# Optimization experiments

Measured on AMD Instinct MI355X. Metric: run time of the kernel, lower is better.

## Reference

```python
import jax, jax.numpy as jnp
import numpy as np
import math

K = 3
K2 = 9
BANDS = 8

def _linear(x, w, b):
    return x @ w.T + b

def _gelu(x):
    return jax.nn.gelu(x, approximate=False)

def setup_inputs() -> dict:
    key = jax.random.key(0)
    ks = jax.random.split(key, 14)
    def p(k, shape):
        return jax.random.normal(k, shape, dtype=jnp.float32) * 0.05
    inp = {
        "feat": jax.random.normal(ks[0], (2, 64, 128, 128), dtype=jnp.float32),
        "w1m": p(ks[1], (64, 85)),  "b1m": p(ks[2], (64,)),
        "w2m": p(ks[3], (64, 64)),  "b2m": p(ks[4], (64,)),
        "wk1": p(ks[5], (128, 640)), "bk1": p(ks[6], (128,)),
        "wk2": p(ks[7], (9, 128)),   "bk2": p(ks[8], (9,)),
        "wr1": p(ks[9], (64, 64)),   "br1": p(ks[10], (64,)),
        "wr2": p(ks[11], (3, 64)),   "br2": p(ks[12], (3,)),
        "scale": 2,
    }
    return inp

def reference(feat, w1m, b1m, w2m, b2m, wk1, bk1, wk2, bk2, wr1, br1, wr2, br2, scale):
    B, C, H, W = feat.shape
    s = float(scale)
    oh = max(1, int(round(H * s)))
    ow = max(1, int(round(W * s)))
    kappa = max(0.1, 1.0 / s)
    eta = min(1.0, 0.15 * s)
    pad = K // 2

    # ---- query geometry (shared across batch: uniform scale) ----
    ys = jnp.arange(oh, dtype=feat.dtype)
    xs = jnp.arange(ow, dtype=feat.dtype)
    yy, xx = jnp.meshgrid(ys, xs, indexing='ij')
    src_y = (yy + 0.5) / s - 0.5
    src_x = (xx + 0.5) / s - 0.5
    cell_y = jnp.floor(src_y)
    cell_x = jnp.floor(src_x)
    du = (src_x - cell_x - 0.5).reshape(-1)  # (q,)
    dv = (src_y - cell_y - 0.5).reshape(-1)
    q = oh * ow

    # ---- gather local KxK patches (replicates unfold + index_select) ----
    cy = jnp.clip(cell_y, 0, H - 1).astype(jnp.int32).reshape(-1)
    cx = jnp.clip(cell_x, 0, W - 1).astype(jnp.int32).reshape(-1)
    padded = jnp.pad(feat, ((0, 0), (0, 0), (pad, pad), (pad, pad)), mode='reflect')
    off = jnp.arange(K, dtype=jnp.int32)
    rows = cy[:, None] + off                 # (q, K) -> padded row indices
    cols = cx[:, None] + off                 # (q, K)
    # (B, C, q, K, K)
    g = padded[:, :, rows[:, :, None], cols[:, None, :]]
    g = jnp.transpose(g, (0, 2, 1, 3, 4)).reshape(B, q, C * K2)  # torch unfold layout (c, kh, kw)
    # torch does gathered.view(q, k2, c) on the channel-major flat -> faithful reshape
    patches = g.reshape(B, q, K2, C)
    patches_flat = g  # (B, q, C*K2), identical to patches.reshape(q, -1)

    # ---- meta fourier encoding + meta MLP (shared across batch) ----
    m = jnp.stack([
        jnp.full((q,), s, dtype=feat.dtype),
        du, dv,
        jnp.full((q,), kappa, dtype=feat.dtype),
        jnp.full((q,), eta, dtype=feat.dtype),
    ], axis=1)                               # (q, 5)
    freqs = (2.0 ** jnp.arange(BANDS, dtype=feat.dtype)) * math.pi
    xb = m[..., None] * freqs                # (q, 5, BANDS)
    enc = jnp.concatenate([m[..., None], jnp.sin(xb), jnp.cos(xb)], axis=-1).reshape(q, -1)  # (q, 85)
    m_emb = _linear(_gelu(_linear(enc, w1m, b1m)), w2m, b2m)  # (q, channels)

    # ---- kernel generation + softmax-weighted aggregate ----
    m_emb_b = jnp.broadcast_to(m_emb[None], (B, q, m_emb.shape[-1]))
    kin = jnp.concatenate([patches_flat, m_emb_b], axis=-1)   # (B, q, 640)
    weights = _linear(_gelu(_linear(kin, wk1, bk1)), wk2, bk2)  # (B, q, K2)
    weights = jax.nn.softmax(weights, axis=-1)
    f_q = jnp.einsum('bqk,bqkc->bqc', weights, patches)       # (B, q, C)

    # ---- rgb head ----
    rgb = _linear(_gelu(_linear(f_q, wr1, br1)), wr2, br2)    # (B, q, 3)
    rgb = rgb.reshape(B, oh, ow, -1).transpose(0, 3, 1, 2)    # (B, 3, oh, ow)
    return rgb
```

## Files before the change

kernel.cpp:

```cpp
#include <hip/hip_runtime.h>
#include <math.h>

#define HH 128
#define WW 128

typedef __attribute__((ext_vector_type(8))) short s16x8;
typedef __attribute__((ext_vector_type(8))) _Float16 h16x8;
typedef __attribute__((ext_vector_type(4))) float f32x4;

__device__ __forceinline__ float gelu_f(float x){
    return 0.5f * x * (1.0f + erff(x * 0.70710678118654752440f));
}
__device__ __forceinline__ float gelu_fast(float x){
    const float u2 = 1.5957691216057308f * x * (1.0f + 0.044715f * x * x);
    const float e  = __expf(u2);
    const float t  = 1.0f - 2.0f / (e + 1.0f);
    return 0.5f * x * (1.0f + t);
}
__device__ __forceinline__ int refl(int v, int n){
    return v < 0 ? -v : (v >= n ? 2*n - 2 - v : v);
}
__device__ __forceinline__ ushort f2bf(float f){
    unsigned int b = __float_as_uint(f);
    unsigned int r = (b + 0x7FFFu + ((b >> 16) & 1u)) >> 16;
    return (ushort)r;
}
__device__ __forceinline__ float bf2f(ushort u){
    return __uint_as_float(((unsigned int)u) << 16);
}

__global__ __launch_bounds__(256) void featTp_kernel(
    const float* __restrict__ feat, ushort* __restrict__ featTp)
{
    const int i = blockIdx.x * 256 + threadIdx.x;
    if (i >= 270400) return;
    const int cb  = i & 7;
    const int col = (i >> 3) % 130;
    const int row = (i / 1040) % 130;
    const int b   = i / 135200;

    const int sr = refl(row - 1, HH);
    const int sc = refl(col - 1, WW);
    const float* __restrict__ src = feat + ((size_t)(b*64 + cb*8) << 14) + (sr << 7) + sc;
    ushort tmp[8];
    #pragma unroll
    for (int j = 0; j < 8; ++j) tmp[j] = f2bf(src[(size_t)j << 14]);
    ushort* dst = featTp + ((((size_t)b*130 + row)*130 + col) << 6) + cb*8;
    *(int4*)dst = *(const int4*)tmp;
}

__global__ __launch_bounds__(256) void prep_all(
    const float* __restrict__ w1m, const float* __restrict__ b1m,
    const float* __restrict__ w2m, const float* __restrict__ b2m,
    const float* __restrict__ wk1, const float* __restrict__ bk1,
    const float* __restrict__ wr1,
    float* __restrict__ contrib, ushort* __restrict__ wk1tap,
    _Float16* __restrict__ wr1h)
{
    const int blk = blockIdx.x;
    const int t = threadIdx.x;

    if (blk == 0){
        __shared__ float hs[4][64];
        __shared__ float m_emb[4][64];
        const int p = t >> 6;
        const int j = t & 63;

        const float du = (p & 1) ? -0.25f : 0.25f;
        const float dv = (p >> 1) ? -0.25f : 0.25f;
        const float mv[5] = {2.0f, du, dv, 0.5f, 0.3f};

        float enc[85];
        #pragma unroll
        for (int f = 0; f < 5; ++f){
            enc[f*17] = mv[f];
            float fr = 3.14159265358979323846f;
            #pragma unroll
            for (int b = 0; b < 8; ++b){
                float xb = mv[f] * fr;
                enc[f*17 + 1 + b] = sinf(xb);
                enc[f*17 + 9 + b] = cosf(xb);
                fr *= 2.0f;
            }
        }

        float h = b1m[j];
        const float* __restrict__ wrow = w1m + j*85;
        #pragma unroll
        for (int i = 0; i < 85; ++i) h += enc[i] * wrow[i];
        hs[p][j] = gelu_f(h);
        __syncthreads();

        {
            const int o = j;
            float acc = b2m[o];
            const float* __restrict__ w2row = w2m + o*64;
            #pragma unroll
            for (int jj = 0; jj < 64; ++jj) acc += hs[p][jj] * w2row[jj];
            m_emb[p][o] = acc;
        }
        __syncthreads();

        for (int e = t; e < 512; e += 256){
            const int pp = e >> 7;
            const int oo = e & 127;
            float a = bk1[oo];
            #pragma unroll
            for (int jj = 0; jj < 64; ++jj) a += m_emb[pp][jj] * wk1[oo*640 + 576 + jj];
            contrib[e] = a;
        }
    } else if (blk <= 288){
        const int i = (blk - 1)*256 + t;
        if (i < 73728){
            const int c   = i & 63;
            const int o   = (i >> 6) & 127;
            const int tap = i >> 13;
            wk1tap[i] = f2bf(wk1[o*640 + c*9 + tap]);
        }
    } else {
        const int i = (blk - 289)*256 + t;
        if (i < 8192) wr1h[i] = (_Float16)wr1[i];
    }
}

__global__ __launch_bounds__(512) void conv_kernel(
    const ushort* __restrict__ featTp,
    const ushort* __restrict__ wk1tap,
    const float* __restrict__ wk2, const float* __restrict__ bk2,
    const float* __restrict__ contrib,
    _Float16* __restrict__ fqh)
{
    __shared__ ushort As[4*34*64];
    __shared__ float  Ls[64][129];
    __shared__ float  wk2s[1152];
    __shared__ float  w9s[256*9];
    __shared__ ushort tbl[576];

    const int t   = threadIdx.x;
    const int blk = blockIdx.x;
    const int b   = blk >> 8;
    const int rem = blk & 255;
    const int cy0 = (rem >> 2) * 2;
    const int cx0 = (rem & 3) * 32;

    for (int e = t; e < 1088; e += 512){
        const int r   = e / 272;
        const int rm  = e - r * 272;
        const int col = rm >> 3;
        const int cb  = rm & 7;
        const ushort* src = featTp + ((((size_t)b*130 + cy0 + r)*130 + cx0 + col) << 6) + cb*8;
        const int didx = (r*34 + col)*64 + ((cb ^ (col & 7)) << 3);
        *(int4*)&As[didx] = *(const int4*)src;
    }
    for (int e = t; e < 1152; e += 512) wk2s[e] = wk2[e];
    for (int e = t; e < 576; e += 512){
        const int ch  = e / 9;
        const int tap = e - 9*ch;
        const int ty  = tap / 3;
        const int tx  = tap - 3*ty;
        tbl[e] = (ushort)((ch << 9) | ((ty*34 + tx) << 2) | tx);
    }
    __syncthreads();

    {
        const int lane = t & 63;
        const int w    = t >> 6;
        const int wn   = w & 1;
        const int wq   = w >> 1;
        const int cellrow = wq >> 1;
        const int colblk  = (wq & 1) * 16;
        const int l15  = lane & 15;
        const int l4   = lane >> 4;

        f32x4 acc[4];
        #pragma unroll
        for (int n = 0; n < 4; ++n) acc[n] = (f32x4){0.f,0.f,0.f,0.f};

        const int acol = colblk + l15;

        #pragma unroll
        for (int tap = 0; tap < 9; ++tap){
            const int ky = tap / 3;
            const int kx = tap - ky * 3;

            s16x8 bf[2][4];
            #pragma unroll
            for (int ks = 0; ks < 2; ++ks)
                #pragma unroll
                for (int n = 0; n < 4; ++n)
                    bf[ks][n] = *(const s16x8*)(wk1tap +
                        (((size_t)tap << 13) + ((wn*64 + n*16 + l15) << 6) + ks*32 + l4*8));

            const int col = acol + kx;
            const int rowbase = (cellrow + ky)*34 + col;
            const int sw = (col & 7);
            #pragma unroll
            for (int ks = 0; ks < 2; ++ks){
                const int cb0 = ks*4 + l4;
                const s16x8 af = *(const s16x8*)&As[rowbase*64 + ((cb0 ^ sw) << 3)];
                #pragma unroll
                for (int n = 0; n < 4; ++n)
                    acc[n] = __builtin_amdgcn_mfma_f32_16x16x32_bf16(af, bf[ks][n], acc[n], 0, 0, 0);
            }
        }

        #pragma unroll
        for (int n = 0; n < 4; ++n){
            #pragma unroll
            for (int reg = 0; reg < 4; ++reg){
                const int lc = cellrow*32 + colblk + l4*4 + reg;
                const int o  = wn*64 + n*16 + l15;
                Ls[lc][o] = acc[n][reg];
            }
        }
    }
    __syncthreads();

    {
        const int task = t >> 1;
        const int half = t & 1;
        const int lc   = task >> 2;
        const int p    = task & 3;

        float w9[9];
        #pragma unroll
        for (int k = 0; k < 9; ++k) w9[k] = 0.0f;

        const int rot = (p*16 + half*8) & 63;
        for (int ii = 0; ii < 64; ++ii){
            const int o = half*64 + ((rot + ii) & 63);
            const float h = gelu_fast(Ls[lc][o] + contrib[p*128 + o]);
            #pragma unroll
            for (int k = 0; k < 9; ++k) w9[k] += wk2s[k*128 + o] * h;
        }
        #pragma unroll
        for (int k = 0; k < 9; ++k) w9[k] += __shfl_xor(w9[k], 1);
        #pragma unroll
        for (int k = 0; k < 9; ++k) w9[k] += bk2[k];

        float mx = w9[0];
        #pragma unroll
        for (int k = 1; k < 9; ++k) mx = fmaxf(mx, w9[k]);
        float sum = 0.0f;
        #pragma unroll
        for (int k = 0; k < 9; ++k){ w9[k] = __expf(w9[k] - mx); sum += w9[k]; }
        const float inv = 1.0f / sum;
        #pragma unroll
        for (int k = 0; k < 9; ++k) w9[k] *= inv;

        if (half == 0){
            w9s[task*9+0] = w9[0]; w9s[task*9+1] = w9[1]; w9s[task*9+2] = w9[2];
            w9s[task*9+3] = w9[3]; w9s[task*9+4] = w9[4];
        } else {
            w9s[task*9+5] = w9[5]; w9s[task*9+6] = w9[6];
            w9s[task*9+7] = w9[7]; w9s[task*9+8] = w9[8];
        }
    }
    __syncthreads();

    {
        const int ci  = t >> 3;
        const int sub = t & 7;
        const int rr  = ci >> 5;
        const int x   = ci & 31;
        const int base_rc = rr*34 + x;
        const int c0 = sub*8;

        float w9r[4][9];
        #pragma unroll
        for (int p = 0; p < 4; ++p)
            #pragma unroll
            for (int k = 0; k < 9; ++k)
                w9r[p][k] = w9s[(ci*4 + p)*9 + k];

        float fqa[4][8];
        #pragma unroll
        for (int p = 0; p < 4; ++p)
            #pragma unroll
            for (int i = 0; i < 8; ++i) fqa[p][i] = 0.0f;

        #pragma unroll
        for (int k = 0; k < 9; ++k){
            #pragma unroll
            for (int i = 0; i < 8; ++i){
                const int e  = tbl[k*64 + c0 + i];
                const int tx = e & 3;
                const int rc = (e >> 2) & 127;
                const int ch = e >> 9;
                const int col = x + tx;
                const int aidx = ((base_rc + rc) << 6)
                               + (((ch >> 3) ^ (col & 7)) << 3) + (ch & 7);
                const float v = bf2f(As[aidx]);
                fqa[0][i] += w9r[0][k] * v;
                fqa[1][i] += w9r[1][k] * v;
                fqa[2][i] += w9r[2][k] * v;
                fqa[3][i] += w9r[3][k] * v;
            }
        }

        const int gy = cy0 + rr;
        const int gx = cx0 + x;

        #pragma unroll
        for (int p = 0; p < 4; ++p){
            const int py = p >> 1, px = p & 1;
            h16x8 hv;
            #pragma unroll
            for (int i = 0; i < 8; ++i) hv[i] = (_Float16)fqa[p][i];

            const int oy0 = 2*gy + 2 - py;
            const int ox0 = 2*gx + 2 - px;
            const bool y0ok = (py == 1) || (gy < 127);
            const bool x0ok = (px == 1) || (gx < 127);
            const bool yEx  = (gy == 0) && (py == 0);
            const bool xEx  = (gx == 0) && (px == 0);

            if (y0ok && x0ok)
                *(h16x8*)(fqh + (((size_t)((b << 16) | (oy0 << 8) | ox0)) << 6) + c0) = hv;
            if (y0ok && xEx)
                *(h16x8*)(fqh + (((size_t)((b << 16) | (oy0 << 8))) << 6) + c0) = hv;
            if (yEx && x0ok)
                *(h16x8*)(fqh + (((size_t)((b << 16) | ox0)) << 6) + c0) = hv;
            if (yEx && xEx)
                *(h16x8*)(fqh + (((size_t)(b << 16)) << 6) + c0) = hv;
        }
    }
}

__global__ __launch_bounds__(256) void rgb_kernel(
    const _Float16* __restrict__ fqh,
    const _Float16* __restrict__ wr1h,
    const float* __restrict__ br1, const float* __restrict__ wr2,
    const float* __restrict__ br2,
    float* __restrict__ out)
{
    const int t    = threadIdx.x;
    const int w    = t >> 6;
    const int lane = t & 63;
    const int l15  = lane & 15;
    const int l4   = lane >> 4;
    const int rowbase = blockIdx.x*64 + w*16;

    const h16x8 a0 = *(const h16x8*)&fqh[(size_t)(rowbase + l15)*64 + l4*8];
    const h16x8 a1 = *(const h16x8*)&fqh[(size_t)(rowbase + l15)*64 + 32 + l4*8];

    f32x4 acc[4];
    #pragma unroll
    for (int n = 0; n < 4; ++n){
        const h16x8 b0 = *(const h16x8*)&wr1h[(n*16 + l15)*64 + l4*8];
        const h16x8 b1 = *(const h16x8*)&wr1h[(n*16 + l15)*64 + 32 + l4*8];
        acc[n] = (f32x4){0.f,0.f,0.f,0.f};
        acc[n] = __builtin_amdgcn_mfma_f32_16x16x32_f16(a0, b0, acc[n], 0, 0, 0);
        acc[n] = __builtin_amdgcn_mfma_f32_16x16x32_f16(a1, b1, acc[n], 0, 0, 0);
    }

    f32x4 br1v, wv0, wv1, wv2;
    #pragma unroll
    for (int n = 0; n < 4; ++n){
        const int col = n*16 + l15;
        br1v[n] = br1[col];
        wv0[n]  = wr2[col];
        wv1[n]  = wr2[64 + col];
        wv2[n]  = wr2[128 + col];
    }
    const float b2r0 = br2[0], b2r1 = br2[1], b2r2 = br2[2];

    #pragma unroll
    for (int reg = 0; reg < 4; ++reg){
        float r0 = 0.f, r1 = 0.f, r2 = 0.f;
        #pragma unroll
        for (int n = 0; n < 4; ++n){
            const float h = gelu_fast(acc[n][reg] + br1v[n]);
            r0 += h * wv0[n];
            r1 += h * wv1[n];
            r2 += h * wv2[n];
        }
        r0 += __shfl_xor(r0, 1); r0 += __shfl_xor(r0, 2); r0 += __shfl_xor(r0, 4); r0 += __shfl_xor(r0, 8);
        r1 += __shfl_xor(r1, 1); r1 += __shfl_xor(r1, 2); r1 += __shfl_xor(r1, 4); r1 += __shfl_xor(r1, 8);
        r2 += __shfl_xor(r2, 1); r2 += __shfl_xor(r2, 2); r2 += __shfl_xor(r2, 4); r2 += __shfl_xor(r2, 8);

        if (l15 == 0){
            const int row = rowbase + l4*4 + reg;
            const int b   = row >> 16;
            const int pix = row & 65535;
            out[((size_t)(b*3 + 0) << 16) + pix] = r0 + b2r0;
            out[((size_t)(b*3 + 1) << 16) + pix] = r1 + b2r1;
            out[((size_t)(b*3 + 2) << 16) + pix] = r2 + b2r2;
        }
    }
}

__global__ __launch_bounds__(256) void main_kernel_mono(
    const float* __restrict__ feat,
    const float* __restrict__ wk1,
    const float* __restrict__ wk2, const float* __restrict__ bk2,
    const float* __restrict__ wr1, const float* __restrict__ br1,
    const float* __restrict__ wr2, const float* __restrict__ br2,
    const float* __restrict__ contrib,
    float* __restrict__ out)
{
    const int tid = blockIdx.x * 256 + threadIdx.x;
    const int b  = tid >> 16;
    const int qi = tid & 65535;
    const int oy = qi >> 8;
    const int ox = qi & 255;

    int cy = (oy - 1) >> 1; if (cy < 0) cy = 0;
    int cx = (ox - 1) >> 1; if (cx < 0) cx = 0;

    int ry[3], rx[3];
    #pragma unroll
    for (int k = 0; k < 3; ++k){ ry[k] = refl(cy-1+k, HH); rx[k] = refl(cx-1+k, WW); }

    const int p = ((oy & 1) << 1) | (ox & 1);
    const float* __restrict__ fb = feat + ((size_t)b << 20);

    float w9[9];
    #pragma unroll
    for (int k = 0; k < 9; ++k) w9[k] = bk2[k];

    for (int oc = 0; oc < 4; ++oc){
        float acc[32];
        #pragma unroll
        for (int j = 0; j < 32; ++j) acc[j] = contrib[p*128 + oc*32 + j];
        for (int c = 0; c < 64; ++c){
            const float* __restrict__ fc = fb + c * (HH*WW);
            float v[9];
            #pragma unroll
            for (int ky = 0; ky < 3; ++ky){
                const float* __restrict__ frow = fc + ry[ky] * WW;
                #pragma unroll
                for (int kx = 0; kx < 3; ++kx) v[ky*3 + kx] = frow[rx[kx]];
            }
            const float* __restrict__ wrow0 = wk1 + (oc*32) * 640 + c * 9;
            #pragma unroll
            for (int j = 0; j < 32; ++j){
                const float* __restrict__ wrow = wrow0 + j * 640;
                float a = acc[j];
                #pragma unroll
                for (int kk = 0; kk < 9; ++kk) a += v[kk] * wrow[kk];
                acc[j] = a;
            }
        }
        #pragma unroll
        for (int j = 0; j < 32; ++j){
            const float h = gelu_f(acc[j]);
            const int o = oc*32 + j;
            #pragma unroll
            for (int k = 0; k < 9; ++k) w9[k] += h * wk2[k*128 + o];
        }
    }

    float mx = w9[0];
    #pragma unroll
    for (int k = 1; k < 9; ++k) mx = fmaxf(mx, w9[k]);
    float sum = 0.0f;
    #pragma unroll
    for (int k = 0; k < 9; ++k){ w9[k] = expf(w9[k] - mx); sum += w9[k]; }
    const float inv = 1.0f / sum;
    #pragma unroll
    for (int k = 0; k < 9; ++k) w9[k] *= inv;

    float fq[64];
    #pragma unroll
    for (int c = 0; c < 64; ++c){
        float a = 0.0f;
        #pragma unroll
        for (int k = 0; k < 9; ++k){
            const int j  = k*64 + c;
            const int ch = j / 9;
            const int kk = j % 9;
            a += w9[k] * fb[ch*(HH*WW) + ry[kk/3]*WW + rx[kk%3]];
        }
        fq[c] = a;
    }

    float r0 = br2[0], r1 = br2[1], r2 = br2[2];
    for (int o = 0; o < 64; ++o){
        float a = br1[o];
        #pragma unroll
        for (int c = 0; c < 64; ++c) a += fq[c] * wr1[o*64 + c];
        const float h = gelu_f(a);
        r0 += h * wr2[o];
        r1 += h * wr2[64 + o];
        r2 += h * wr2[128 + o];
    }

    const int pix = (oy << 8) | ox;
    out[((size_t)(b*3 + 0) << 16) + pix] = r0;
    out[((size_t)(b*3 + 1) << 16) + pix] = r1;
    out[((size_t)(b*3 + 2) << 16) + pix] = r2;
}

extern "C" void kernel_launch(void* const* d_in, const int* in_sizes, int n_in,
                              void* d_out, int out_size, void* d_ws, size_t ws_size,
                              hipStream_t stream)
{
    const float* feat = (const float*)d_in[0];
    const float* w1m  = (const float*)d_in[1];
    const float* b1m  = (const float*)d_in[2];
    const float* w2m  = (const float*)d_in[3];
    const float* b2m  = (const float*)d_in[4];
    const float* wk1  = (const float*)d_in[5];
    const float* bk1  = (const float*)d_in[6];
    const float* wk2  = (const float*)d_in[7];
    const float* bk2  = (const float*)d_in[8];
    const float* wr1  = (const float*)d_in[9];
    const float* br1  = (const float*)d_in[10];
    const float* wr2  = (const float*)d_in[11];
    const float* br2  = (const float*)d_in[12];

    float* out = (float*)d_out;

    char* ws = (char*)d_ws;
    float*     contrib = (float*)ws;
    ushort*    wk1tap  = (ushort*)(ws + 8192);
    _Float16*  wr1h    = (_Float16*)(ws + 155648);
    ushort*    featTp  = (ushort*)(ws + 172032);
    _Float16*  fqh     = (_Float16*)(ws + 4498432);
    const size_t need = 21275648;

    hipLaunchKernelGGL(prep_all, dim3(321), dim3(256), 0, stream,
                       w1m, b1m, w2m, b2m, wk1, bk1, wr1, contrib, wk1tap, wr1h);

    if (ws_size >= need){
        hipLaunchKernelGGL(featTp_kernel, dim3(1057), dim3(256), 0, stream, feat, featTp);
        hipLaunchKernelGGL(conv_kernel, dim3(512), dim3(512), 0, stream,
                           featTp, wk1tap, wk2, bk2, contrib, fqh);
        hipLaunchKernelGGL(rgb_kernel, dim3(2048), dim3(256), 0, stream,
                           fqh, wr1h, br1, wr2, br2, out);
    } else {
        hipLaunchKernelGGL(main_kernel_mono, dim3(512), dim3(256), 0, stream,
                           feat, wk1, wk2, bk2, wr1, br1, wr2, br2, contrib, out);
    }
}
```

Measured before the change: 184.5 us.

## Tile featTp transpose through LDS and restructure conv kernel epilogue stages

The pad/transpose kernel now stages one padded row of all 64 channels in shared memory, so global reads are coalesced along columns, and then writes channel-packed bf16 vectors. The launch shrinks from 1057 to 260 blocks. In the conv kernel, the hidden activations are stored to LDS as fp16 to cut LDS footprint, and wk2 is transposed so each step loads it as float4 vectors. The 9-tap reduction now uses 256 threads, one per query, with no shuffle. The tap lookup table is replaced by multiply-shift index arithmetic, and divisions in GELU and softmax use hardware reciprocal. The trade-offs are lower precision in the intermediate activations and only half the threads active in the softmax stage.

```diff
diff --git a/kernel.cpp b/kernel.cpp
--- a/kernel.cpp
+++ b/kernel.cpp
@@ -11,10 +11,10 @@
 __device__ __forceinline__ float gelu_f(float x){
     return 0.5f * x * (1.0f + erff(x * 0.70710678118654752440f));
 }
-__device__ __forceinline__ float gelu_fast(float x){
+__device__ __forceinline__ float gelu2(float x){
     const float u2 = 1.5957691216057308f * x * (1.0f + 0.044715f * x * x);
     const float e  = __expf(u2);
-    const float t  = 1.0f - 2.0f / (e + 1.0f);
+    const float t  = 1.0f - 2.0f * __builtin_amdgcn_rcpf(e + 1.0f);
     return 0.5f * x * (1.0f + t);
 }
 __device__ __forceinline__ int refl(int v, int n){
@@ -32,21 +32,36 @@
 __global__ __launch_bounds__(256) void featTp_kernel(
     const float* __restrict__ feat, ushort* __restrict__ featTp)
 {
-    const int i = blockIdx.x * 256 + threadIdx.x;
-    if (i >= 270400) return;
-    const int cb  = i & 7;
-    const int col = (i >> 3) % 130;
-    const int row = (i / 1040) % 130;
-    const int b   = i / 135200;
-
-    const int sr = refl(row - 1, HH);
-    const int sc = refl(col - 1, WW);
-    const float* __restrict__ src = feat + ((size_t)(b*64 + cb*8) << 14) + (sr << 7) + sc;
-    ushort tmp[8];
-    #pragma unroll
-    for (int j = 0; j < 8; ++j) tmp[j] = f2bf(src[(size_t)j << 14]);
-    ushort* dst = featTp + ((((size_t)b*130 + row)*130 + col) << 6) + cb*8;
-    *(int4*)dst = *(const int4*)tmp;
+    __shared__ ushort tile[64*132];
+
+    const int blk = blockIdx.x;
+    const int b   = blk / 130;
+    const int row = blk - b*130;
+    const int sr  = refl(row - 1, HH);
+
+    const int c2   = threadIdx.x >> 7;
+    const int scol = threadIdx.x & 127;
+
+    #pragma unroll 4
+    for (int cc = 0; cc < 32; ++cc){
+        const int c = cc*2 + c2;
+        const float v = feat[(((size_t)(b*64 + c)) << 14) + (sr << 7) + scol];
+        const ushort bv = f2bf(v);
+        tile[c*132 + scol + 1] = bv;
+        if (scol == 1)   tile[c*132 + 0]   = bv;
+        if (scol == 126) tile[c*132 + 129] = bv;
+    }
+    __syncthreads();
+
+    for (int e = threadIdx.x; e < 1040; e += 256){
+        const int col = e >> 3;
+        const int cb  = e & 7;
+        ushort tmp[8];
+        #pragma unroll
+        for (int j = 0; j < 8; ++j) tmp[j] = tile[(cb*8 + j)*132 + col];
+        *(int4*)(featTp + ((((size_t)b*130 + row)*130 + col) << 6) + cb*8)
+            = *(const int4*)tmp;
+    }
 }
 
 __global__ __launch_bounds__(256) void prep_all(
@@ -131,10 +146,10 @@
     _Float16* __restrict__ fqh)
 {
     __shared__ ushort As[4*34*64];
-    __shared__ float  Ls[64][129];
-    __shared__ float  wk2s[1152];
-    __shared__ float  w9s[256*9];
-    __shared__ ushort tbl[576];
+    __shared__ ushort Ls16[64*130];
+    __shared__ float  wk2t[128*12];
+    __shared__ float  w9s[256*10];
+    __shared__ float  contribs[512];
 
     const int t   = threadIdx.x;
     const int blk = blockIdx.x;
@@ -152,14 +167,12 @@
         const int didx = (r*34 + col)*64 + ((cb ^ (col & 7)) << 3);
         *(int4*)&As[didx] = *(const int4*)src;
     }
-    for (int e = t; e < 1152; e += 512) wk2s[e] = wk2[e];
-    for (int e = t; e < 576; e += 512){
-        const int ch  = e / 9;
-        const int tap = e - 9*ch;
-        const int ty  = tap / 3;
-        const int tx  = tap - 3*ty;
-        tbl[e] = (ushort)((ch << 9) | ((ty*34 + tx) << 2) | tx);
-    }
+    for (int e = t; e < 1536; e += 512){
+        const int o = (e * 10923) >> 17;
+        const int k = e - o*12;
+        if (k < 9) wk2t[e] = wk2[k*128 + o];
+    }
+    if (t < 512) contribs[t] = contrib[t];
     __syncthreads();
 
     {
@@ -210,31 +223,30 @@
             for (int reg = 0; reg < 4; ++reg){
                 const int lc = cellrow*32 + colblk + l4*4 + reg;
                 const int o  = wn*64 + n*16 + l15;
-                Ls[lc][o] = acc[n][reg];
+                Ls16[lc*130 + o] = __builtin_bit_cast(ushort, (_Float16)acc[n][reg]);
             }
         }
     }
     __syncthreads();
 
-    {
-        const int task = t >> 1;
-        const int half = t & 1;
-        const int lc   = task >> 2;
-        const int p    = task & 3;
+    if (t < 256){
+        const int cell = t & 63;
+        const int p    = t >> 6;
 
         float w9[9];
         #pragma unroll
         for (int k = 0; k < 9; ++k) w9[k] = 0.0f;
 
-        const int rot = (p*16 + half*8) & 63;
-        for (int ii = 0; ii < 64; ++ii){
-            const int o = half*64 + ((rot + ii) & 63);
-            const float h = gelu_fast(Ls[lc][o] + contrib[p*128 + o]);
-            #pragma unroll
-            for (int k = 0; k < 9; ++k) w9[k] += wk2s[k*128 + o] * h;
-        }
-        #pragma unroll
-        for (int k = 0; k < 9; ++k) w9[k] += __shfl_xor(w9[k], 1);
+        const float* __restrict__ cp = contribs + p*128;
+        for (int o = 0; o < 128; ++o){
+            const float lv = (float)__builtin_bit_cast(_Float16, Ls16[cell*130 + o]);
+            const float h  = gelu2(lv + cp[o]);
+            const f32x4 wa = *(const f32x4*)&wk2t[o*12];
+            const f32x4 wb = *(const f32x4*)&wk2t[o*12 + 4];
+            w9[0] += h*wa[0]; w9[1] += h*wa[1]; w9[2] += h*wa[2]; w9[3] += h*wa[3];
+            w9[4] += h*wb[0]; w9[5] += h*wb[1]; w9[6] += h*wb[2]; w9[7] += h*wb[3];
+            w9[8] += h*wk2t[o*12 + 8];
+        }
         #pragma unroll
         for (int k = 0; k < 9; ++k) w9[k] += bk2[k];
 
@@ -244,17 +256,9 @@
         float sum = 0.0f;
         #pragma unroll
         for (int k = 0; k < 9; ++k){ w9[k] = __expf(w9[k] - mx); sum += w9[k]; }
-        const float inv = 1.0f / sum;
-        #pragma unroll
-        for (int k = 0; k < 9; ++k) w9[k] *= inv;
-
-        if (half == 0){
-            w9s[task*9+0] = w9[0]; w9s[task*9+1] = w9[1]; w9s[task*9+2] = w9[2];
-            w9s[task*9+3] = w9[3]; w9s[task*9+4] = w9[4];
-        } else {
-            w9s[task*9+5] = w9[5]; w9s[task*9+6] = w9[6];
-            w9s[task*9+7] = w9[7]; w9s[task*9+8] = w9[8];
-        }
+        const float inv = __builtin_amdgcn_rcpf(sum);
+        #pragma unroll
+        for (int k = 0; k < 9; ++k) w9s[t*10 + k] = w9[k] * inv;
     }
     __syncthreads();
 
@@ -271,7 +275,7 @@
         for (int p = 0; p < 4; ++p)
             #pragma unroll
             for (int k = 0; k < 9; ++k)
-                w9r[p][k] = w9s[(ci*4 + p)*9 + k];
+                w9r[p][k] = w9s[(p*64 + ci)*10 + k];
 
         float fqa[4][8];
         #pragma unroll
@@ -283,12 +287,13 @@
         for (int k = 0; k < 9; ++k){
             #pragma unroll
             for (int i = 0; i < 8; ++i){
-                const int e  = tbl[k*64 + c0 + i];
-                const int tx = e & 3;
-                const int rc = (e >> 2) & 127;
-                const int ch = e >> 9;
+                const int e   = k*64 + c0 + i;
+                const int ch  = (e * 7282) >> 16;
+                const int tap = e - 9*ch;
+                const int ty  = (tap * 11) >> 5;
+                const int tx  = tap - 3*ty;
                 const int col = x + tx;
-                const int aidx = ((base_rc + rc) << 6)
+                const int aidx = ((base_rc + ty*34 + tx) << 6)
                                + (((ch >> 3) ^ (col & 7)) << 3) + (ch & 7);
                 const float v = bf2f(As[aidx]);
                 fqa[0][i] += w9r[0][k] * v;
@@ -370,7 +375,7 @@
         float r0 = 0.f, r1 = 0.f, r2 = 0.f;
         #pragma unroll
         for (int n = 0; n < 4; ++n){
-            const float h = gelu_fast(acc[n][reg] + br1v[n]);
+            const float h = gelu2(acc[n][reg] + br1v[n]);
             r0 += h * wv0[n];
             r1 += h * wv1[n];
             r2 += h * wv2[n];
@@ -524,7 +529,7 @@
                        w1m, b1m, w2m, b2m, wk1, bk1, wr1, contrib, wk1tap, wr1h);
 
     if (ws_size >= need){
-        hipLaunchKernelGGL(featTp_kernel, dim3(1057), dim3(256), 0, stream, feat, featTp);
+        hipLaunchKernelGGL(featTp_kernel, dim3(260), dim3(256), 0, stream, feat, featTp);
         hipLaunchKernelGGL(conv_kernel, dim3(512), dim3(512), 0, stream,
                            featTp, wk1tap, wk2, bk2, contrib, fqh);
         hipLaunchKernelGGL(rgb_kernel, dim3(2048), dim3(256), 0, stream,
```

Measured after the change: 184.2 us. No clear change (-0.2%).
